# Optimization experiments

Measured on AMD Instinct MI355X. Metric: run time of the kernel, lower is better.

Reference implementation:

```python
import jax, jax.numpy as jnp
import numpy as np

B, BEV = 2, 128
Q = BEV * BEV          # 16384 BEV queries
C, H, L, P = 256, 8, 1, 4
D = C // H             # 32 per-head dim


def setup_inputs() -> dict:
    key = jax.random.key(0)
    ks = jax.random.split(key, 14)
    s = 0.02
    return {
        "query": jax.random.normal(ks[0], (B, Q, C), jnp.float32),
        "value": jax.random.normal(ks[1], (B, Q, C), jnp.float32),
        "identity": jax.random.normal(ks[2], (B, Q, C), jnp.float32),
        "query_pos": jax.random.normal(ks[3], (B, Q, C), jnp.float32),
        "reference_points": jax.random.uniform(ks[4], (B, Q, L, 2), jnp.float32),
        "spatial_shapes": jnp.array([[BEV, BEV]], jnp.int32),
        "level_start_index": jnp.array([0], jnp.int32),
        "Wv": jax.random.normal(ks[5], (C, C), jnp.float32) * s,
        "bv": jnp.zeros((C,), jnp.float32),
        "Woff": jax.random.normal(ks[6], (C, H * L * P * 2), jnp.float32) * s,
        "boff": jax.random.normal(ks[7], (H * L * P * 2,), jnp.float32) * s,
        "Ww": jax.random.normal(ks[8], (C, H * L * P), jnp.float32) * s,
        "bw": jnp.zeros((H * L * P,), jnp.float32),
        "Wo": jax.random.normal(ks[9], (C, C), jnp.float32) * s,
        "bo": jnp.zeros((C,), jnp.float32),
    }


def _deform_attn(q, v, reference_points, shapes_np, Wv, bv, Woff, boff, Ww, bw, Wo, bo):
    b, nq, _ = q.shape
    v = v @ Wv + bv                                             # value_proj
    off = (q @ Woff + boff).reshape(b, nq, H, L, P, 2)          # sampling offsets
    attn = jax.nn.softmax((q @ Ww + bw).reshape(b, nq, H, L * P), axis=-1)
    attn = attn.reshape(b, nq, H, L, P)
    # offset normalizer is (W, H) per level
    norm = jnp.asarray(shapes_np[:, ::-1], jnp.float32)         # [L, 2]
    loc = reference_points[:, :, None, :, None, :] + off / norm[None, None, None, :, None, :]

    out = jnp.zeros((b, H, nq, D), jnp.float32)
    start = 0
    for l in range(L):
        Hl, Wl = int(shapes_np[l, 0]), int(shapes_np[l, 1])
        N = Hl * Wl
        vl = v[:, start:start + N].reshape(b, N, H, D).transpose(0, 2, 1, 3)  # [b,H,N,D]
        start += N
        ll = loc[:, :, :, l]                                    # [b,nq,H,P,2] in [0,1]
        # grid_sample(align_corners=False): pixel coord = loc*size - 0.5
        x = ll[..., 0] * Wl - 0.5
        y = ll[..., 1] * Hl - 0.5
        x0 = jnp.floor(x); y0 = jnp.floor(y)
        dx = x - x0; dy = y - y0
        x0i = x0.astype(jnp.int32); y0i = y0.astype(jnp.int32)

        def gather(ix, iy):
            valid = (ix >= 0) & (ix < Wl) & (iy >= 0) & (iy < Hl)  # zero padding
            idx = jnp.clip(iy, 0, Hl - 1) * Wl + jnp.clip(ix, 0, Wl - 1)
            idx = idx.transpose(0, 2, 1, 3).reshape(b, H, nq * P)
            g = jnp.take_along_axis(vl, idx[..., None], axis=2)   # [b,H,nq*P,D]
            return g * valid.transpose(0, 2, 1, 3).reshape(b, H, nq * P, 1)

        def cw(w):  # corner weight -> [b,H,nq*P,1]
            return w.transpose(0, 2, 1, 3).reshape(b, H, nq * P, 1)

        samp = (gather(x0i, y0i) * cw((1 - dx) * (1 - dy))
                + gather(x0i + 1, y0i) * cw(dx * (1 - dy))
                + gather(x0i, y0i + 1) * cw((1 - dx) * dy)
                + gather(x0i + 1, y0i + 1) * cw(dx * dy))
        samp = samp.reshape(b, H, nq, P, D)
        aw = attn[:, :, :, l].transpose(0, 2, 1, 3)             # [b,H,nq,P]
        out = out + jnp.einsum('bhqpd,bhqp->bhqd', samp, aw)

    out = out.transpose(0, 2, 1, 3).reshape(b, nq, C)
    return out @ Wo + bo                                        # output_proj


def reference(query, value, identity, query_pos, reference_points, spatial_shapes,
              level_start_index, Wv, bv, Woff, boff, Ww, bw, Wo, bo):
    shapes_np = np.asarray(spatial_shapes)                      # static level shapes
    q = query + query_pos
    out = _deform_attn(q, value, reference_points, shapes_np,
                       Wv, bv, Woff, boff, Ww, bw, Wo, bo)
    return out + identity
```

## Files before the change

kernel.cpp:

```cpp
#include <hip/hip_runtime.h>
#include <hip/hip_bf16.h>
#include <stdint.h>

#define Q_TOT 32768
#define CC 256
#define GRID_W 128
#define GRID_H 128

typedef __attribute__((ext_vector_type(8))) short short8;
typedef __attribute__((ext_vector_type(4))) float floatx4;

__device__ __forceinline__ ushort f2bf(float f) {
    union { float f; uint32_t u; } v; v.f = f;
    uint32_t r = (v.u + 0x7fffu + ((v.u >> 16) & 1u)) >> 16;
    return (ushort)r;
}
__device__ __forceinline__ float bf2f(ushort s) {
    union { uint32_t u; float f; } v; v.u = ((uint32_t)s) << 16;
    return v.f;
}
__device__ __forceinline__ void bf2x2(uint32_t u, float& lo, float& hi) {
    union { uint32_t u; float f; } a, b;
    a.u = u << 16; b.u = u & 0xffff0000u;
    lo = a.f; hi = b.f;
}
__device__ __forceinline__ void async_load16(const void* g, void* l) {
    __builtin_amdgcn_global_load_lds(
        reinterpret_cast<const __attribute__((address_space(1))) uint32_t*>(
            reinterpret_cast<uintptr_t>(g)),
        reinterpret_cast<__attribute__((address_space(3))) uint32_t*>(
            reinterpret_cast<uintptr_t>(l)),
        16, 0, 0);
}

__global__ __launch_bounds__(256)
void prep_convert(const float* __restrict__ q, const float* __restrict__ qp,
                  const float* __restrict__ val,
                  ushort* __restrict__ qsum, ushort* __restrict__ vbf)
{
    const int total = (Q_TOT * CC) / 4;
    for (int idx = blockIdx.x * blockDim.x + threadIdx.x; idx < 2 * total;
         idx += gridDim.x * blockDim.x) {
        if (idx < total) {
            float4 a = ((const float4*)q)[idx];
            float4 b = ((const float4*)qp)[idx];
            ushort4 o;
            o.x = f2bf(a.x + b.x); o.y = f2bf(a.y + b.y);
            o.z = f2bf(a.z + b.z); o.w = f2bf(a.w + b.w);
            ((ushort4*)qsum)[idx] = o;
        } else {
            int j = idx - total;
            float4 a = ((const float4*)val)[j];
            ushort4 o;
            o.x = f2bf(a.x); o.y = f2bf(a.y); o.z = f2bf(a.z); o.w = f2bf(a.w);
            ((ushort4*)vbf)[j] = o;
        }
    }
}

__global__ __launch_bounds__(256)
void prep_weights(const float* __restrict__ Wv, const float* __restrict__ Wo,
                  const float* __restrict__ Woff, const float* __restrict__ Ww,
                  const float* __restrict__ boff, const float* __restrict__ bw,
                  ushort* __restrict__ WvT, ushort* __restrict__ WoT,
                  ushort* __restrict__ WowT, float* __restrict__ bias_ow)
{
    int idx = blockIdx.x * blockDim.x + threadIdx.x;
    if (idx < 65536) {
        int n = idx >> 8, k = idx & 255;
        WvT[idx] = f2bf(Wv[k * 256 + n]);
    } else if (idx < 131072) {
        int t = idx - 65536; int n = t >> 8, k = t & 255;
        WoT[t] = f2bf(Wo[k * 256 + n]);
    } else if (idx < 155648) {
        int t = idx - 131072; int n = t >> 8, k = t & 255;
        float v = (n < 64) ? Woff[k * 64 + n] : Ww[k * 32 + (n - 64)];
        WowT[t] = f2bf(v);
    } else if (idx < 155744) {
        int t = idx - 155648;
        bias_ow[t] = (t < 64) ? boff[t] : bw[t - 64];
    }
}

template <int BM, int BN, int WAVE_M, int WAVE_N, bool OUT_BF16>
__global__ __launch_bounds__(256)
void gemm_bf16(const ushort* __restrict__ A, const ushort* __restrict__ Bt,
               const float* __restrict__ bias, const float* __restrict__ res,
               void* __restrict__ Cout, int M, int N, int K)
{
    constexpr int TM = BM / WAVE_M / 16;
    constexpr int TN = BN / WAVE_N / 16;
    __shared__ ushort As[BM * 32];
    __shared__ ushort Bs[BN * 32];

    const int tid = threadIdx.x;
    const int lane = tid & 63;
    const int wave = tid >> 6;
    const int wm = wave / WAVE_N;
    const int wn = wave % WAVE_N;
    const int quad = lane >> 4;
    const int m16 = lane & 15;
    const int lrow = lane >> 2;
    const int lkk = (lane & 3) * 8;

    const int row0 = blockIdx.y * BM;
    const int col0 = blockIdx.x * BN;

    floatx4 acc[TM][TN] = {};

    for (int k0 = 0; k0 < K; k0 += 32) {
        #pragma unroll
        for (int i = wave; i < BM / 16; i += 4) {
            const ushort* src = A + (size_t)(row0 + i * 16 + lrow) * K + (k0 + lkk);
            async_load16(src, &As[i * 16 * 32]);
        }
        #pragma unroll
        for (int i = wave; i < BN / 16; i += 4) {
            const ushort* src = Bt + (size_t)(col0 + i * 16 + lrow) * K + (k0 + lkk);
            async_load16(src, &Bs[i * 16 * 32]);
        }
        __syncthreads();

        short8 af[TM], bf[TN];
        #pragma unroll
        for (int i = 0; i < TM; ++i)
            af[i] = *(const short8*)&As[(wm * TM * 16 + i * 16 + m16) * 32 + quad * 8];
        #pragma unroll
        for (int j = 0; j < TN; ++j)
            bf[j] = *(const short8*)&Bs[(wn * TN * 16 + j * 16 + m16) * 32 + quad * 8];
        #pragma unroll
        for (int i = 0; i < TM; ++i)
            #pragma unroll
            for (int j = 0; j < TN; ++j)
                acc[i][j] = __builtin_amdgcn_mfma_f32_16x16x32_bf16(
                    af[i], bf[j], acc[i][j], 0, 0, 0);
        __syncthreads();
    }

    #pragma unroll
    for (int i = 0; i < TM; ++i) {
        #pragma unroll
        for (int j = 0; j < TN; ++j) {
            const int gcol = col0 + wn * TN * 16 + j * 16 + m16;
            const float bb = bias[gcol];
            #pragma unroll
            for (int r = 0; r < 4; ++r) {
                const int grow = row0 + wm * TM * 16 + i * 16 + quad * 4 + r;
                float v = acc[i][j][r] + bb;
                if (res) v += res[(size_t)grow * N + gcol];
                if constexpr (OUT_BF16)
                    ((ushort*)Cout)[(size_t)grow * N + gcol] = f2bf(v);
                else
                    ((float*)Cout)[(size_t)grow * N + gcol] = v;
            }
        }
    }
}

#define QB 8
__global__ __launch_bounds__(256)
void sample_kernel(const ushort* __restrict__ v2,
                   const ushort* __restrict__ ow,
                   const float* __restrict__ ref,
                   ushort* __restrict__ out)
{
    const int tid = threadIdx.x;
    const int ql = tid >> 5;
    const int h  = (tid >> 2) & 7;
    const int dg = tid & 3;
    const int q = blockIdx.x * QB + ql;
    const int b = q >> 14;

    const ushort* op = ow + (size_t)q * 96 + h * 8;
    const uint4 oraw = *(const uint4*)op;
    float offs[8];
    bf2x2(oraw.x, offs[0], offs[1]);
    bf2x2(oraw.y, offs[2], offs[3]);
    bf2x2(oraw.z, offs[4], offs[5]);
    bf2x2(oraw.w, offs[6], offs[7]);

    const uint2 wraw = *(const uint2*)(ow + (size_t)q * 96 + 64 + h * 4);
    float w0, w1, w2, w3;
    bf2x2(wraw.x, w0, w1);
    bf2x2(wraw.y, w2, w3);
    float m = fmaxf(fmaxf(w0, w1), fmaxf(w2, w3));
    float e0 = __expf(w0 - m), e1 = __expf(w1 - m), e2 = __expf(w2 - m), e3 = __expf(w3 - m);
    float inv = 1.f / (e0 + e1 + e2 + e3);
    float aw[4] = {e0 * inv, e1 * inv, e2 * inv, e3 * inv};

    const float rx = ref[(size_t)q * 2 + 0];
    const float ry = ref[(size_t)q * 2 + 1];
    const ushort* vb = v2 + (size_t)b * 16384 * 256 + h * 32 + dg * 8;

    float acc[8] = {};
    #pragma unroll
    for (int p = 0; p < 4; ++p) {
        float x = rx * (float)GRID_W + offs[p * 2 + 0] - 0.5f;
        float y = ry * (float)GRID_H + offs[p * 2 + 1] - 0.5f;
        float x0f = floorf(x), y0f = floorf(y);
        float dx = x - x0f, dy = y - y0f;
        int x0 = (int)x0f, y0 = (int)y0f;
        int x1 = x0 + 1, y1 = y0 + 1;
        float vx0 = (x0 >= 0 && x0 < GRID_W) ? 1.f : 0.f;
        float vx1 = (x1 >= 0 && x1 < GRID_W) ? 1.f : 0.f;
        float vy0 = (y0 >= 0 && y0 < GRID_H) ? 1.f : 0.f;
        float vy1 = (y1 >= 0 && y1 < GRID_H) ? 1.f : 0.f;
        int xc0 = min(max(x0, 0), GRID_W - 1), xc1 = min(max(x1, 0), GRID_W - 1);
        int yc0 = min(max(y0, 0), GRID_H - 1), yc1 = min(max(y1, 0), GRID_H - 1);
        float cw00 = aw[p] * (1.f - dx) * (1.f - dy) * vx0 * vy0;
        float cw10 = aw[p] * dx * (1.f - dy) * vx1 * vy0;
        float cw01 = aw[p] * (1.f - dx) * dy * vx0 * vy1;
        float cw11 = aw[p] * dx * dy * vx1 * vy1;
        const int base0 = yc0 * GRID_W, base1 = yc1 * GRID_W;
        const uint4 r00 = *(const uint4*)(vb + (size_t)(base0 + xc0) * 256);
        const uint4 r10 = *(const uint4*)(vb + (size_t)(base0 + xc1) * 256);
        const uint4 r01 = *(const uint4*)(vb + (size_t)(base1 + xc0) * 256);
        const uint4 r11 = *(const uint4*)(vb + (size_t)(base1 + xc1) * 256);
        float lo, hi;
        bf2x2(r00.x, lo, hi); acc[0] += cw00 * lo; acc[1] += cw00 * hi;
        bf2x2(r00.y, lo, hi); acc[2] += cw00 * lo; acc[3] += cw00 * hi;
        bf2x2(r00.z, lo, hi); acc[4] += cw00 * lo; acc[5] += cw00 * hi;
        bf2x2(r00.w, lo, hi); acc[6] += cw00 * lo; acc[7] += cw00 * hi;
        bf2x2(r10.x, lo, hi); acc[0] += cw10 * lo; acc[1] += cw10 * hi;
        bf2x2(r10.y, lo, hi); acc[2] += cw10 * lo; acc[3] += cw10 * hi;
        bf2x2(r10.z, lo, hi); acc[4] += cw10 * lo; acc[5] += cw10 * hi;
        bf2x2(r10.w, lo, hi); acc[6] += cw10 * lo; acc[7] += cw10 * hi;
        bf2x2(r01.x, lo, hi); acc[0] += cw01 * lo; acc[1] += cw01 * hi;
        bf2x2(r01.y, lo, hi); acc[2] += cw01 * lo; acc[3] += cw01 * hi;
        bf2x2(r01.z, lo, hi); acc[4] += cw01 * lo; acc[5] += cw01 * hi;
        bf2x2(r01.w, lo, hi); acc[6] += cw01 * lo; acc[7] += cw01 * hi;
        bf2x2(r11.x, lo, hi); acc[0] += cw11 * lo; acc[1] += cw11 * hi;
        bf2x2(r11.y, lo, hi); acc[2] += cw11 * lo; acc[3] += cw11 * hi;
        bf2x2(r11.z, lo, hi); acc[4] += cw11 * lo; acc[5] += cw11 * hi;
        bf2x2(r11.w, lo, hi); acc[6] += cw11 * lo; acc[7] += cw11 * hi;
    }

    uint4 o;
    o.x = ((uint32_t)f2bf(acc[1]) << 16) | f2bf(acc[0]);
    o.y = ((uint32_t)f2bf(acc[3]) << 16) | f2bf(acc[2]);
    o.z = ((uint32_t)f2bf(acc[5]) << 16) | f2bf(acc[4]);
    o.w = ((uint32_t)f2bf(acc[7]) << 16) | f2bf(acc[6]);
    *(uint4*)(out + (size_t)q * 256 + h * 32 + dg * 8) = o;
}

extern "C" void kernel_launch(void* const* d_in, const int* in_sizes, int n_in,
                              void* d_out, int out_size, void* d_ws, size_t ws_size,
                              hipStream_t stream) {
    const float* query     = (const float*)d_in[0];
    const float* value     = (const float*)d_in[1];
    const float* identity  = (const float*)d_in[2];
    const float* query_pos = (const float*)d_in[3];
    const float* refpts    = (const float*)d_in[4];
    const float* Wv   = (const float*)d_in[7];
    const float* bv   = (const float*)d_in[8];
    const float* Woff = (const float*)d_in[9];
    const float* boff = (const float*)d_in[10];
    const float* Ww   = (const float*)d_in[11];
    const float* bw   = (const float*)d_in[12];
    const float* Wo   = (const float*)d_in[13];
    const float* bo   = (const float*)d_in[14];
    float* out = (float*)d_out;

    char* ws = (char*)d_ws;
    ushort* qsum_bf  = (ushort*)(ws);
    ushort* value_bf = (ushort*)(ws + 16777216);
    ushort* v2_bf    = (ushort*)(ws + 33554432);
    ushort* ow_bf    = (ushort*)(ws + 50331648);
    ushort* samp_bf  = (ushort*)(ws + 56623104);
    ushort* WvT      = (ushort*)(ws + 73400320);
    ushort* WoT      = (ushort*)(ws + 73531392);
    ushort* WowT     = (ushort*)(ws + 73662464);
    float*  bias_ow  = (float*)(ws + 73711616);

    prep_convert<<<8192, 256, 0, stream>>>(query, query_pos, value, qsum_bf, value_bf);
    prep_weights<<<609, 256, 0, stream>>>(Wv, Wo, Woff, Ww, boff, bw,
                                          WvT, WoT, WowT, bias_ow);
    gemm_bf16<128, 128, 2, 2, true><<<dim3(2, 256), 256, 0, stream>>>(
        value_bf, WvT, bv, nullptr, v2_bf, Q_TOT, 256, 256);
    gemm_bf16<64, 96, 4, 1, true><<<dim3(1, 512), 256, 0, stream>>>(
        qsum_bf, WowT, bias_ow, nullptr, ow_bf, Q_TOT, 96, 256);
    sample_kernel<<<dim3(Q_TOT / QB), 256, 0, stream>>>(v2_bf, ow_bf, refpts, samp_bf);
    gemm_bf16<128, 128, 2, 2, false><<<dim3(2, 256), 256, 0, stream>>>(
        samp_bf, WoT, bo, identity, out, Q_TOT, 256, 256);
}
```

Baseline: 268.8 us.

## Load full K panel into LDS once per GEMM tile and shrink tiles

```diff
diff --git a/kernel.cpp b/kernel.cpp
--- a/kernel.cpp
+++ b/kernel.cpp
@@ -83,15 +83,20 @@
 }
 
 template <int BM, int BN, int WAVE_M, int WAVE_N, bool OUT_BF16>
-__global__ __launch_bounds__(256)
+__global__ __launch_bounds__(WAVE_M * WAVE_N * 64, 2)
 void gemm_bf16(const ushort* __restrict__ A, const ushort* __restrict__ Bt,
                const float* __restrict__ bias, const float* __restrict__ res,
-               void* __restrict__ Cout, int M, int N, int K)
-{
+               void* __restrict__ Cout, int M, int N)
+{
+    constexpr int K = 256;
+    constexpr int NC = K / 32;
+    constexpr int NW = WAVE_M * WAVE_N;
+    constexpr int GA = BM / 16;
+    constexpr int GB = BN / 16;
     constexpr int TM = BM / WAVE_M / 16;
     constexpr int TN = BN / WAVE_N / 16;
-    __shared__ ushort As[BM * 32];
-    __shared__ ushort Bs[BN * 32];
+    __shared__ ushort As[BM * K];
+    __shared__ ushort Bs[BN * K];
 
     const int tid = threadIdx.x;
     const int lane = tid & 63;
@@ -106,46 +111,49 @@
     const int row0 = blockIdx.y * BM;
     const int col0 = blockIdx.x * BN;
 
+    #pragma unroll
+    for (int t = 0; t < (NC * GA) / NW; ++t) {
+        const int idx = t * NW + wave;
+        const int c = idx / GA, g = idx % GA;
+        const ushort* src = A + (size_t)(row0 + g * 16 + lrow) * K + c * 32 + lkk;
+        async_load16(src, &As[(c * GA + g) * 512]);
+    }
+    #pragma unroll
+    for (int t = 0; t < (NC * GB) / NW; ++t) {
+        const int idx = t * NW + wave;
+        const int c = idx / GB, g = idx % GB;
+        const ushort* src = Bt + (size_t)(col0 + g * 16 + lrow) * K + c * 32 + lkk;
+        async_load16(src, &Bs[(c * GB + g) * 512]);
+    }
+    __syncthreads();
+
     floatx4 acc[TM][TN] = {};
-
-    for (int k0 = 0; k0 < K; k0 += 32) {
-        #pragma unroll
-        for (int i = wave; i < BM / 16; i += 4) {
-            const ushort* src = A + (size_t)(row0 + i * 16 + lrow) * K + (k0 + lkk);
-            async_load16(src, &As[i * 16 * 32]);
-        }
-        #pragma unroll
-        for (int i = wave; i < BN / 16; i += 4) {
-            const ushort* src = Bt + (size_t)(col0 + i * 16 + lrow) * K + (k0 + lkk);
-            async_load16(src, &Bs[i * 16 * 32]);
-        }
-        __syncthreads();
-
+    #pragma unroll
+    for (int c = 0; c < NC; ++c) {
         short8 af[TM], bf[TN];
         #pragma unroll
         for (int i = 0; i < TM; ++i)
-            af[i] = *(const short8*)&As[(wm * TM * 16 + i * 16 + m16) * 32 + quad * 8];
+            af[i] = *(const short8*)&As[((c * GA + wm * TM + i) * 16 + m16) * 32 + quad * 8];
         #pragma unroll
         for (int j = 0; j < TN; ++j)
-            bf[j] = *(const short8*)&Bs[(wn * TN * 16 + j * 16 + m16) * 32 + quad * 8];
+            bf[j] = *(const short8*)&Bs[((c * GB + wn * TN + j) * 16 + m16) * 32 + quad * 8];
         #pragma unroll
         for (int i = 0; i < TM; ++i)
             #pragma unroll
             for (int j = 0; j < TN; ++j)
                 acc[i][j] = __builtin_amdgcn_mfma_f32_16x16x32_bf16(
                     af[i], bf[j], acc[i][j], 0, 0, 0);
-        __syncthreads();
     }
 
     #pragma unroll
     for (int i = 0; i < TM; ++i) {
         #pragma unroll
         for (int j = 0; j < TN; ++j) {
-            const int gcol = col0 + wn * TN * 16 + j * 16 + m16;
+            const int gcol = col0 + (wn * TN + j) * 16 + m16;
             const float bb = bias[gcol];
             #pragma unroll
             for (int r = 0; r < 4; ++r) {
-                const int grow = row0 + wm * TM * 16 + i * 16 + quad * 4 + r;
+                const int grow = row0 + (wm * TM + i) * 16 + quad * 4 + r;
                 float v = acc[i][j][r] + bb;
                 if (res) v += res[(size_t)grow * N + gcol];
                 if constexpr (OUT_BF16)
@@ -275,11 +283,11 @@
     prep_convert<<<8192, 256, 0, stream>>>(query, query_pos, value, qsum_bf, value_bf);
     prep_weights<<<609, 256, 0, stream>>>(Wv, Wo, Woff, Ww, boff, bw,
                                           WvT, WoT, WowT, bias_ow);
-    gemm_bf16<128, 128, 2, 2, true><<<dim3(2, 256), 256, 0, stream>>>(
-        value_bf, WvT, bv, nullptr, v2_bf, Q_TOT, 256, 256);
-    gemm_bf16<64, 96, 4, 1, true><<<dim3(1, 512), 256, 0, stream>>>(
-        qsum_bf, WowT, bias_ow, nullptr, ow_bf, Q_TOT, 96, 256);
+    gemm_bf16<64, 64, 2, 2, true><<<dim3(4, 512), 256, 0, stream>>>(
+        value_bf, WvT, bv, nullptr, v2_bf, Q_TOT, 256);
+    gemm_bf16<64, 96, 2, 2, true><<<dim3(1, 512), 256, 0, stream>>>(
+        qsum_bf, WowT, bias_ow, nullptr, ow_bf, Q_TOT, 96);
     sample_kernel<<<dim3(Q_TOT / QB), 256, 0, stream>>>(v2_bf, ow_bf, refpts, samp_bf);
-    gemm_bf16<128, 128, 2, 2, false><<<dim3(2, 256), 256, 0, stream>>>(
-        samp_bf, WoT, bo, identity, out, Q_TOT, 256, 256);
-}
+    gemm_bf16<64, 64, 2, 2, false><<<dim3(4, 512), 256, 0, stream>>>(
+        samp_bf, WoT, bo, identity, out, Q_TOT, 256);
+}
```

After: 271.5 us. No clear change (+1.0%).
